# Kernel tuning notes

Measured on AMD Instinct MI355X. Metric: run time of the kernel, lower is better.

The kernel has to match this reference:

```python
import jax, jax.numpy as jnp
import numpy as np

B, S = 8192, 32
N_NODES, N_EDGES = 200000, 500000
D_NODE = D_EDGE = 172
D_TIME = 100
D_IN = D_NODE + D_NODE + D_EDGE + D_TIME  # 616


def setup_inputs() -> dict:
    key = jax.random.key(0)
    ks = jax.random.split(key, 16)
    node_raw_features = jax.random.normal(ks[0], (N_NODES, D_NODE), dtype=jnp.float32)
    edge_raw_features = jax.random.normal(ks[1], (N_EDGES, D_EDGE), dtype=jnp.float32)
    src_node_ids = jax.random.randint(ks[2], (B,), 0, N_NODES)
    dst_node_ids = jax.random.randint(ks[3], (B,), 0, N_NODES)
    node_interact_times = jax.random.uniform(ks[4], (B,), dtype=jnp.float32) * 1000.0
    src_nbr_ids = jax.random.randint(ks[5], (B, S), 0, N_NODES)
    src_edge_ids = jax.random.randint(ks[6], (B, S), 0, N_EDGES)
    src_nbr_times = jax.random.uniform(ks[7], (B, S), dtype=jnp.float32) * 1000.0
    dst_nbr_ids = jax.random.randint(ks[8], (B, S), 0, N_NODES)
    dst_edge_ids = jax.random.randint(ks[9], (B, S), 0, N_EDGES)
    dst_nbr_times = jax.random.uniform(ks[10], (B, S), dtype=jnp.float32) * 1000.0
    # TimeEncoder: frozen Linear(1, D_TIME) with w = 1/10^linspace(0,9,D_TIME), b = 0
    time_w = (1.0 / (10.0 ** jnp.linspace(0.0, 9.0, D_TIME))).astype(jnp.float32)
    time_b = jnp.zeros((D_TIME,), dtype=jnp.float32)
    W_out = jax.random.normal(ks[11], (D_IN, D_NODE), dtype=jnp.float32) * 0.02
    b_out = jnp.zeros((D_NODE,), dtype=jnp.float32)
    return {
        "node_raw_features": node_raw_features,
        "edge_raw_features": edge_raw_features,
        "src_node_ids": src_node_ids,
        "dst_node_ids": dst_node_ids,
        "node_interact_times": node_interact_times,
        "src_nbr_ids": src_nbr_ids,
        "src_edge_ids": src_edge_ids,
        "src_nbr_times": src_nbr_times,
        "dst_nbr_ids": dst_nbr_ids,
        "dst_edge_ids": dst_edge_ids,
        "dst_nbr_times": dst_nbr_times,
        "time_w": time_w,
        "time_b": time_b,
        "W_out": W_out,
        "b_out": b_out,
    }


def _side_embedding(node_raw_features, edge_raw_features, node_ids, interact_times,
                    nbr_ids, edge_ids, nbr_times, time_w, time_b, W_out, b_out):
    nf = node_raw_features[nbr_ids]            # [B,S,D_NODE] gather
    ef = edge_raw_features[edge_ids]           # [B,S,D_EDGE] gather
    dt = interact_times[:, None] - nbr_times   # [B,S]
    tf = jnp.cos(dt[..., None] * time_w + time_b)  # [B,S,D_TIME]
    tf = jnp.where((nbr_ids == 0)[..., None], 0.0, tf)  # zero padded-time features
    combined = jnp.concatenate([nf, ef, tf], axis=-1)   # [B,S,D_NODE+D_EDGE+D_TIME]
    agg = combined.mean(axis=1)                          # mean over padded seq (divide by S)
    cur = node_raw_features[node_ids]                    # [B,D_NODE]
    inp = jnp.concatenate([cur, agg], axis=-1)           # [B,D_IN]
    return jax.nn.relu(inp @ W_out + b_out)              # dropout is identity in eval


def reference(node_raw_features, edge_raw_features, src_node_ids, dst_node_ids,
              node_interact_times, src_nbr_ids, src_edge_ids, src_nbr_times,
              dst_nbr_ids, dst_edge_ids, dst_nbr_times, time_w, time_b, W_out, b_out):
    src_emb = _side_embedding(node_raw_features, edge_raw_features, src_node_ids,
                              node_interact_times, src_nbr_ids, src_edge_ids,
                              src_nbr_times, time_w, time_b, W_out, b_out)
    dst_emb = _side_embedding(node_raw_features, edge_raw_features, dst_node_ids,
                              node_interact_times, dst_nbr_ids, dst_edge_ids,
                              dst_nbr_times, time_w, time_b, W_out, b_out)
    dummy = jnp.zeros_like(src_emb)
    return src_emb, dst_emb, dummy
```

## Files before the change

### kernel.cpp

```cpp
#include <hip/hip_runtime.h>

#define ROWS  16
#define BLOCK 512
#define PAD   620

__global__ __launch_bounds__(BLOCK) void spe_fused(
    const float* __restrict__ nodef,
    const float* __restrict__ edgef,
    const int*   __restrict__ src_ids,
    const int*   __restrict__ dst_ids,
    const float* __restrict__ itimes,
    const int*   __restrict__ s_nbr,
    const int*   __restrict__ s_eid,
    const float* __restrict__ s_t,
    const int*   __restrict__ d_nbr,
    const int*   __restrict__ d_eid,
    const float* __restrict__ d_t,
    const float* __restrict__ tw,
    const float* __restrict__ tb,
    const float* __restrict__ W,
    const float* __restrict__ bout,
    float*       __restrict__ out)
{
    __shared__ float inp[ROWS * PAD];
    __shared__ int   noff[ROWS * 32];
    __shared__ int   eoff[ROWS * 32];
    __shared__ float dtm[ROWS * 32];
    __shared__ float msk[ROWS * 32];
    __shared__ int   curoff[ROWS];
    __shared__ float twl[100], tbl[100];

    const int tid     = threadIdx.x;
    const int side    = blockIdx.x >> 9;
    const int rowbase = (blockIdx.x & 511) * ROWS;

    const int*   nbr  = side ? d_nbr : s_nbr;
    const int*   eidp = side ? d_eid : s_eid;
    const float* ntp  = side ? d_t   : s_t;
    const int*   nids = side ? dst_ids : src_ids;

    {
        int i   = tid;
        int g   = rowbase * 32 + i;
        int nid = nbr[g];
        noff[i] = nid * 172;
        eoff[i] = eidp[g] * 172;
        dtm[i]  = itimes[rowbase + (i >> 5)] - ntp[g];
        msk[i]  = (nid == 0) ? 0.f : 1.f;
    }
    if (tid < ROWS) curoff[tid] = nids[rowbase + tid] * 172;
    if (tid < 100) { twl[tid] = tw[tid]; tbl[tid] = tb[tid]; }
    __syncthreads();

    for (int i = tid; i < ROWS * 43; i += BLOCK) {
        int r = i / 43, c = i - r * 43;
        *(float4*)&inp[r * PAD + 4 * c] =
            *(const float4*)&nodef[curoff[r] + 4 * c];
    }

    for (int i = tid; i < ROWS * 43; i += BLOCK) {
        int r = i / 43, c = i - r * 43;
        const int dd = 4 * c, rb = r * 32;
        float4 acc = {0.f, 0.f, 0.f, 0.f};
        #pragma unroll
        for (int s0 = 0; s0 < 32; s0 += 8) {
            float4 v[8];
            #pragma unroll
            for (int u = 0; u < 8; ++u)
                v[u] = *(const float4*)&nodef[noff[rb + s0 + u] + dd];
            #pragma unroll
            for (int u = 0; u < 8; ++u) {
                acc.x += v[u].x; acc.y += v[u].y;
                acc.z += v[u].z; acc.w += v[u].w;
            }
        }
        acc.x *= (1.f/32.f); acc.y *= (1.f/32.f);
        acc.z *= (1.f/32.f); acc.w *= (1.f/32.f);
        *(float4*)&inp[r * PAD + 172 + dd] = acc;
    }

    for (int i = tid; i < ROWS * 43; i += BLOCK) {
        int r = i / 43, c = i - r * 43;
        const int dd = 4 * c, rb = r * 32;
        float4 acc = {0.f, 0.f, 0.f, 0.f};
        #pragma unroll
        for (int s0 = 0; s0 < 32; s0 += 8) {
            float4 v[8];
            #pragma unroll
            for (int u = 0; u < 8; ++u)
                v[u] = *(const float4*)&edgef[eoff[rb + s0 + u] + dd];
            #pragma unroll
            for (int u = 0; u < 8; ++u) {
                acc.x += v[u].x; acc.y += v[u].y;
                acc.z += v[u].z; acc.w += v[u].w;
            }
        }
        acc.x *= (1.f/32.f); acc.y *= (1.f/32.f);
        acc.z *= (1.f/32.f); acc.w *= (1.f/32.f);
        *(float4*)&inp[r * PAD + 344 + dd] = acc;
    }

    for (int i = tid; i < ROWS * 100; i += BLOCK) {
        int r = i / 100, j = i - r * 100;
        const int rb = r * 32;
        float w = twl[j], b = tbl[j];
        float acc = 0.f;
        #pragma unroll
        for (int s = 0; s < 32; ++s)
            acc += msk[rb + s] * __cosf(dtm[rb + s] * w + b);
        inp[r * PAD + 516 + j] = acc * (1.f / 32.f);
    }
    __syncthreads();

    if (tid < 344) {
        const int ct = tid % 43, rt = tid / 43;
        const int j0 = ct * 4, r0 = rt * 2;
        float acc[2][4] = {};
        float a[2][4];
        for (int k = 0; k < 616; k += 4) {
            #pragma unroll
            for (int ri = 0; ri < 2; ++ri)
                *(float4*)&a[ri][0] = *(const float4*)&inp[(r0 + ri) * PAD + k];
            #pragma unroll
            for (int kk = 0; kk < 4; ++kk) {
                float4 wv = *(const float4*)&W[(k + kk) * 172 + j0];
                #pragma unroll
                for (int ri = 0; ri < 2; ++ri) {
                    acc[ri][0] += a[ri][kk] * wv.x;
                    acc[ri][1] += a[ri][kk] * wv.y;
                    acc[ri][2] += a[ri][kk] * wv.z;
                    acc[ri][3] += a[ri][kk] * wv.w;
                }
            }
        }
        float4 bias = *(const float4*)&bout[j0];
        #pragma unroll
        for (int ri = 0; ri < 2; ++ri) {
            int row = rowbase + r0 + ri;
            float4 v;
            v.x = fmaxf(acc[ri][0] + bias.x, 0.f);
            v.y = fmaxf(acc[ri][1] + bias.y, 0.f);
            v.z = fmaxf(acc[ri][2] + bias.z, 0.f);
            v.w = fmaxf(acc[ri][3] + bias.w, 0.f);
            *(float4*)&out[(size_t)(side * 8192 + row) * 172 + j0] = v;
        }
    }

    if (side == 0) {
        const float4 z = {0.f, 0.f, 0.f, 0.f};
        for (int i = tid; i < ROWS * 43; i += BLOCK) {
            int r = i / 43, c = i - r * 43;
            *(float4*)&out[(size_t)(2 * 8192 + rowbase + r) * 172 + 4 * c] = z;
        }
    }
}

extern "C" void kernel_launch(void* const* d_in, const int* in_sizes, int n_in,
                              void* d_out, int out_size, void* d_ws, size_t ws_size,
                              hipStream_t stream) {
    const float* nodef   = (const float*)d_in[0];
    const float* edgef   = (const float*)d_in[1];
    const int*   src_ids = (const int*)  d_in[2];
    const int*   dst_ids = (const int*)  d_in[3];
    const float* itimes  = (const float*)d_in[4];
    const int*   s_nbr   = (const int*)  d_in[5];
    const int*   s_eid   = (const int*)  d_in[6];
    const float* s_t     = (const float*)d_in[7];
    const int*   d_nbr   = (const int*)  d_in[8];
    const int*   d_eid   = (const int*)  d_in[9];
    const float* d_t     = (const float*)d_in[10];
    const float* tw      = (const float*)d_in[11];
    const float* tb      = (const float*)d_in[12];
    const float* W       = (const float*)d_in[13];
    const float* bout    = (const float*)d_in[14];
    float* out = (float*)d_out;

    spe_fused<<<1024, BLOCK, 0, stream>>>(
        nodef, edgef, src_ids, dst_ids, itimes,
        s_nbr, s_eid, s_t, d_nbr, d_eid, d_t,
        tw, tb, W, bout, out);
}
```

Before: 221.7 us.

## Split neighbor gather into separate high-parallelism kernel feeding GEMM kernel

Moves the node and edge neighbor gather-mean out of the fused kernel into a separate kernel with one thread per (row, float4 column), launched over 5504 blocks, writing aggregates to workspace. The GEMM kernel then reads the precomputed aggregates instead of performing the gathers. The aim is more memory-level parallelism for the random gathers, which were limited by the fused kernel's 1024 blocks. The cost is an extra workspace round trip and a second launch.

```diff
diff --git a/kernel.cpp b/kernel.cpp
--- a/kernel.cpp
+++ b/kernel.cpp
@@ -1,30 +1,69 @@
 #include <hip/hip_runtime.h>
 
 #define ROWS  16
-#define BLOCK 512
+#define GB    512
+#define PB    256
 #define PAD   620
+#define AGG_STRIDE 344
 
-__global__ __launch_bounds__(BLOCK) void spe_fused(
+__global__ __launch_bounds__(PB) void prep_gather(
     const float* __restrict__ nodef,
     const float* __restrict__ edgef,
+    const int*   __restrict__ s_nbr,
+    const int*   __restrict__ s_eid,
+    const int*   __restrict__ d_nbr,
+    const int*   __restrict__ d_eid,
+    float*       __restrict__ agg)
+{
+    const int i    = blockIdx.x * PB + threadIdx.x;
+    const int grow = i / 86, cc = i - grow * 86;
+    const int side = grow >> 13, row = grow & 8191;
+    const bool is_edge = cc >= 43;
+    const int  c  = is_edge ? cc - 43 : cc;
+    const int  dd = 4 * c;
+
+    const int* idt = is_edge ? (side ? d_eid : s_eid)
+                             : (side ? d_nbr : s_nbr);
+    const float* bp = is_edge ? edgef : nodef;
+    const int4* idv = (const int4*)&idt[row * 32];
+
+    float4 acc = {0.f, 0.f, 0.f, 0.f};
+    #pragma unroll
+    for (int b = 0; b < 4; ++b) {
+        int4 q0 = idv[2 * b], q1 = idv[2 * b + 1];
+        int off[8] = {q0.x, q0.y, q0.z, q0.w, q1.x, q1.y, q1.z, q1.w};
+        float4 v[8];
+        #pragma unroll
+        for (int u = 0; u < 8; ++u)
+            v[u] = *(const float4*)&bp[off[u] * 172 + dd];
+        #pragma unroll
+        for (int u = 0; u < 8; ++u) {
+            acc.x += v[u].x; acc.y += v[u].y;
+            acc.z += v[u].z; acc.w += v[u].w;
+        }
+    }
+    acc.x *= (1.f/32.f); acc.y *= (1.f/32.f);
+    acc.z *= (1.f/32.f); acc.w *= (1.f/32.f);
+    *(float4*)&agg[(size_t)grow * AGG_STRIDE + (is_edge ? 172 : 0) + dd] = acc;
+}
+
+__global__ __launch_bounds__(GB) void gemm_fused(
+    const float* __restrict__ nodef,
     const int*   __restrict__ src_ids,
     const int*   __restrict__ dst_ids,
     const float* __restrict__ itimes,
     const int*   __restrict__ s_nbr,
-    const int*   __restrict__ s_eid,
     const float* __restrict__ s_t,
     const int*   __restrict__ d_nbr,
-    const int*   __restrict__ d_eid,
     const float* __restrict__ d_t,
     const float* __restrict__ tw,
     const float* __restrict__ tb,
     const float* __restrict__ W,
     const float* __restrict__ bout,
+    const float* __restrict__ agg,
     float*       __restrict__ out)
 {
     __shared__ float inp[ROWS * PAD];
-    __shared__ int   noff[ROWS * 32];
-    __shared__ int   eoff[ROWS * 32];
     __shared__ float dtm[ROWS * 32];
     __shared__ float msk[ROWS * 32];
     __shared__ int   curoff[ROWS];
@@ -35,7 +74,6 @@
     const int rowbase = (blockIdx.x & 511) * ROWS;
 
     const int*   nbr  = side ? d_nbr : s_nbr;
-    const int*   eidp = side ? d_eid : s_eid;
     const float* ntp  = side ? d_t   : s_t;
     const int*   nids = side ? dst_ids : src_ids;
 
@@ -43,8 +81,6 @@
         int i   = tid;
         int g   = rowbase * 32 + i;
         int nid = nbr[g];
-        noff[i] = nid * 172;
-        eoff[i] = eidp[g] * 172;
         dtm[i]  = itimes[rowbase + (i >> 5)] - ntp[g];
         msk[i]  = (nid == 0) ? 0.f : 1.f;
     }
@@ -52,55 +88,19 @@
     if (tid < 100) { twl[tid] = tw[tid]; tbl[tid] = tb[tid]; }
     __syncthreads();
 
-    for (int i = tid; i < ROWS * 43; i += BLOCK) {
+    for (int i = tid; i < ROWS * 43; i += GB) {
         int r = i / 43, c = i - r * 43;
         *(float4*)&inp[r * PAD + 4 * c] =
             *(const float4*)&nodef[curoff[r] + 4 * c];
     }
 
-    for (int i = tid; i < ROWS * 43; i += BLOCK) {
-        int r = i / 43, c = i - r * 43;
-        const int dd = 4 * c, rb = r * 32;
-        float4 acc = {0.f, 0.f, 0.f, 0.f};
-        #pragma unroll
-        for (int s0 = 0; s0 < 32; s0 += 8) {
-            float4 v[8];
-            #pragma unroll
-            for (int u = 0; u < 8; ++u)
-                v[u] = *(const float4*)&nodef[noff[rb + s0 + u] + dd];
-            #pragma unroll
-            for (int u = 0; u < 8; ++u) {
-                acc.x += v[u].x; acc.y += v[u].y;
-                acc.z += v[u].z; acc.w += v[u].w;
-            }
-        }
-        acc.x *= (1.f/32.f); acc.y *= (1.f/32.f);
-        acc.z *= (1.f/32.f); acc.w *= (1.f/32.f);
-        *(float4*)&inp[r * PAD + 172 + dd] = acc;
+    for (int i = tid; i < ROWS * 86; i += GB) {
+        int r = i / 86, c = i - r * 86;
+        *(float4*)&inp[r * PAD + 172 + 4 * c] =
+            *(const float4*)&agg[(size_t)(side * 8192 + rowbase + r) * AGG_STRIDE + 4 * c];
     }
 
-    for (int i = tid; i < ROWS * 43; i += BLOCK) {
-        int r = i / 43, c = i - r * 43;
-        const int dd = 4 * c, rb = r * 32;
-        float4 acc = {0.f, 0.f, 0.f, 0.f};
-        #pragma unroll
-        for (int s0 = 0; s0 < 32; s0 += 8) {
-            float4 v[8];
-            #pragma unroll
-            for (int u = 0; u < 8; ++u)
-                v[u] = *(const float4*)&edgef[eoff[rb + s0 + u] + dd];
-            #pragma unroll
-            for (int u = 0; u < 8; ++u) {
-                acc.x += v[u].x; acc.y += v[u].y;
-                acc.z += v[u].z; acc.w += v[u].w;
-            }
-        }
-        acc.x *= (1.f/32.f); acc.y *= (1.f/32.f);
-        acc.z *= (1.f/32.f); acc.w *= (1.f/32.f);
-        *(float4*)&inp[r * PAD + 344 + dd] = acc;
-    }
-
-    for (int i = tid; i < ROWS * 100; i += BLOCK) {
+    for (int i = tid; i < ROWS * 100; i += GB) {
         int r = i / 100, j = i - r * 100;
         const int rb = r * 32;
         float w = twl[j], b = tbl[j];
@@ -148,7 +148,7 @@
 
     if (side == 0) {
         const float4 z = {0.f, 0.f, 0.f, 0.f};
-        for (int i = tid; i < ROWS * 43; i += BLOCK) {
+        for (int i = tid; i < ROWS * 43; i += GB) {
             int r = i / 43, c = i - r * 43;
             *(float4*)&out[(size_t)(2 * 8192 + rowbase + r) * 172 + 4 * c] = z;
         }
@@ -174,9 +174,13 @@
     const float* W       = (const float*)d_in[13];
     const float* bout    = (const float*)d_in[14];
     float* out = (float*)d_out;
+    float* agg = (float*)d_ws;
 
-    spe_fused<<<1024, BLOCK, 0, stream>>>(
-        nodef, edgef, src_ids, dst_ids, itimes,
-        s_nbr, s_eid, s_t, d_nbr, d_eid, d_t,
-        tw, tb, W, bout, out);
+    prep_gather<<<5504, PB, 0, stream>>>(
+        nodef, edgef, s_nbr, s_eid, d_nbr, d_eid, agg);
+
+    gemm_fused<<<1024, GB, 0, stream>>>(
+        nodef, src_ids, dst_ids, itimes,
+        s_nbr, s_t, d_nbr, d_t,
+        tw, tb, W, bout, agg, out);
 }
```

Result: slower. 258.8 us (+16.8%).

## Quantize feature tables to FP8 and split fused kernel into gather stages

Applied to the files above, without the earlier changes.

Splits the single fused kernel into separate passes: quantize the node and edge tables to FP8 in workspace, then gather and mean-reduce neighbour features from the FP8 copies. The current-node copy, the time encoding and the final GEMM each become their own kernel, all going through an fp32 intermediate buffer. The goal is to shrink the bytes moved by the random neighbour gathers. In exchange, every call reads both full tables to quantize them, adds an intermediate round trip and several launches, and FP8 rounding may loosen accuracy.

```diff
diff --git a/kernel.cpp b/kernel.cpp
--- a/kernel.cpp
+++ b/kernel.cpp
@@ -1,114 +1,150 @@
 #include <hip/hip_runtime.h>
 
-#define ROWS  16
-#define BLOCK 512
-#define PAD   620
-
-__global__ __launch_bounds__(BLOCK) void spe_fused(
+typedef float v2f __attribute__((ext_vector_type(2)));
+
+#define NROWS_GRID 16
+#define GB 512
+
+__device__ inline unsigned pack4_fp8(float a, float b, float c, float d) {
+    int t = __builtin_amdgcn_cvt_pk_fp8_f32(a, b, 0, false);
+    t     = __builtin_amdgcn_cvt_pk_fp8_f32(c, d, t, true);
+    return (unsigned)t;
+}
+
+__global__ __launch_bounds__(256) void quant_tab(
+    const float* __restrict__ src,
+    uint4*       __restrict__ dst,
+    int n)
+{
+    int i = blockIdx.x * 256 + threadIdx.x;
+    int row = i / 11, c = i - row * 11;
+    if (row >= n) return;
+    const float4* s = (const float4*)(src + (size_t)row * 172);
+    float v[16];
+    if (c < 10) {
+        #pragma unroll
+        for (int j = 0; j < 4; ++j) {
+            float4 f = s[4 * c + j];
+            v[4*j+0] = f.x; v[4*j+1] = f.y; v[4*j+2] = f.z; v[4*j+3] = f.w;
+        }
+    } else {
+        #pragma unroll
+        for (int j = 0; j < 3; ++j) {
+            float4 f = s[40 + j];
+            v[4*j+0] = f.x; v[4*j+1] = f.y; v[4*j+2] = f.z; v[4*j+3] = f.w;
+        }
+        v[12] = v[13] = v[14] = v[15] = 0.f;
+    }
+    uint4 o;
+    o.x = pack4_fp8(v[0],  v[1],  v[2],  v[3]);
+    o.y = pack4_fp8(v[4],  v[5],  v[6],  v[7]);
+    o.z = pack4_fp8(v[8],  v[9],  v[10], v[11]);
+    o.w = pack4_fp8(v[12], v[13], v[14], v[15]);
+    dst[(size_t)row * 11 + c] = o;
+}
+
+__global__ __launch_bounds__(256) void gather_q(
+    const uint4* __restrict__ Q,
+    const int*   __restrict__ s_ids,
+    const int*   __restrict__ d_ids,
+    float*       __restrict__ inpw,
+    int baseoff)
+{
+    int i    = blockIdx.x * 256 + threadIdx.x;
+    int grow = i / 11, c = i - grow * 11;
+    int side = grow >> 13, row = grow & 8191;
+    const int4* idv = (const int4*)&((side ? d_ids : s_ids)[row * 32]);
+
+    float acc[16];
+    #pragma unroll
+    for (int k = 0; k < 16; ++k) acc[k] = 0.f;
+
+    #pragma unroll
+    for (int b = 0; b < 4; ++b) {
+        int4 q0 = idv[2 * b], q1 = idv[2 * b + 1];
+        int off[8] = {q0.x, q0.y, q0.z, q0.w, q1.x, q1.y, q1.z, q1.w};
+        uint4 v[8];
+        #pragma unroll
+        for (int u = 0; u < 8; ++u)
+            v[u] = Q[(size_t)off[u] * 11 + c];
+        #pragma unroll
+        for (int u = 0; u < 8; ++u) {
+            unsigned w[4] = {v[u].x, v[u].y, v[u].z, v[u].w};
+            #pragma unroll
+            for (int q = 0; q < 4; ++q) {
+                v2f lo = __builtin_amdgcn_cvt_pk_f32_fp8((int)w[q], false);
+                v2f hi = __builtin_amdgcn_cvt_pk_f32_fp8((int)w[q], true);
+                acc[4*q+0] += lo.x; acc[4*q+1] += lo.y;
+                acc[4*q+2] += hi.x; acc[4*q+3] += hi.y;
+            }
+        }
+    }
+
+    float* dstrow = inpw + (size_t)grow * 616 + baseoff + 16 * c;
+    int nf4 = (c == 10) ? 3 : 4;
+    for (int j = 0; j < nf4; ++j) {
+        float4 o = { acc[4*j+0] * (1.f/32.f), acc[4*j+1] * (1.f/32.f),
+                     acc[4*j+2] * (1.f/32.f), acc[4*j+3] * (1.f/32.f) };
+        *(float4*)(dstrow + 4 * j) = o;
+    }
+}
+
+__global__ __launch_bounds__(256) void cur_copy(
     const float* __restrict__ nodef,
-    const float* __restrict__ edgef,
     const int*   __restrict__ src_ids,
     const int*   __restrict__ dst_ids,
+    float*       __restrict__ inpw)
+{
+    int i    = blockIdx.x * 256 + threadIdx.x;
+    int grow = i / 43, c = i - grow * 43;
+    int side = grow >> 13, row = grow & 8191;
+    int id   = (side ? dst_ids : src_ids)[row];
+    *(float4*)(inpw + (size_t)grow * 616 + 4 * c) =
+        *(const float4*)(nodef + (size_t)id * 172 + 4 * c);
+}
+
+__global__ __launch_bounds__(256) void time_enc(
+    const int*   __restrict__ s_nbr,
+    const int*   __restrict__ d_nbr,
+    const float* __restrict__ s_t,
+    const float* __restrict__ d_t,
     const float* __restrict__ itimes,
-    const int*   __restrict__ s_nbr,
-    const int*   __restrict__ s_eid,
-    const float* __restrict__ s_t,
-    const int*   __restrict__ d_nbr,
-    const int*   __restrict__ d_eid,
-    const float* __restrict__ d_t,
     const float* __restrict__ tw,
     const float* __restrict__ tb,
+    float*       __restrict__ inpw)
+{
+    int i    = blockIdx.x * 256 + threadIdx.x;
+    int grow = i / 100, j = i - grow * 100;
+    int side = grow >> 13, row = grow & 8191;
+    const int*   nbr = (side ? d_nbr : s_nbr) + row * 32;
+    const float* nt  = (side ? d_t   : s_t)   + row * 32;
+    float it = itimes[row];
+    float w = tw[j], b = tb[j];
+    float acc = 0.f;
+    #pragma unroll
+    for (int s = 0; s < 32; ++s) {
+        float m = (nbr[s] == 0) ? 0.f : 1.f;
+        acc += m * __cosf((it - nt[s]) * w + b);
+    }
+    inpw[(size_t)grow * 616 + 516 + j] = acc * (1.f / 32.f);
+}
+
+__global__ __launch_bounds__(GB) void final_gemm(
+    const float* __restrict__ inpw,
     const float* __restrict__ W,
     const float* __restrict__ bout,
     float*       __restrict__ out)
 {
-    __shared__ float inp[ROWS * PAD];
-    __shared__ int   noff[ROWS * 32];
-    __shared__ int   eoff[ROWS * 32];
-    __shared__ float dtm[ROWS * 32];
-    __shared__ float msk[ROWS * 32];
-    __shared__ int   curoff[ROWS];
-    __shared__ float twl[100], tbl[100];
-
-    const int tid     = threadIdx.x;
-    const int side    = blockIdx.x >> 9;
-    const int rowbase = (blockIdx.x & 511) * ROWS;
-
-    const int*   nbr  = side ? d_nbr : s_nbr;
-    const int*   eidp = side ? d_eid : s_eid;
-    const float* ntp  = side ? d_t   : s_t;
-    const int*   nids = side ? dst_ids : src_ids;
-
-    {
-        int i   = tid;
-        int g   = rowbase * 32 + i;
-        int nid = nbr[g];
-        noff[i] = nid * 172;
-        eoff[i] = eidp[g] * 172;
-        dtm[i]  = itimes[rowbase + (i >> 5)] - ntp[g];
-        msk[i]  = (nid == 0) ? 0.f : 1.f;
-    }
-    if (tid < ROWS) curoff[tid] = nids[rowbase + tid] * 172;
-    if (tid < 100) { twl[tid] = tw[tid]; tbl[tid] = tb[tid]; }
-    __syncthreads();
-
-    for (int i = tid; i < ROWS * 43; i += BLOCK) {
-        int r = i / 43, c = i - r * 43;
-        *(float4*)&inp[r * PAD + 4 * c] =
-            *(const float4*)&nodef[curoff[r] + 4 * c];
-    }
-
-    for (int i = tid; i < ROWS * 43; i += BLOCK) {
-        int r = i / 43, c = i - r * 43;
-        const int dd = 4 * c, rb = r * 32;
-        float4 acc = {0.f, 0.f, 0.f, 0.f};
-        #pragma unroll
-        for (int s0 = 0; s0 < 32; s0 += 8) {
-            float4 v[8];
-            #pragma unroll
-            for (int u = 0; u < 8; ++u)
-                v[u] = *(const float4*)&nodef[noff[rb + s0 + u] + dd];
-            #pragma unroll
-            for (int u = 0; u < 8; ++u) {
-                acc.x += v[u].x; acc.y += v[u].y;
-                acc.z += v[u].z; acc.w += v[u].w;
-            }
-        }
-        acc.x *= (1.f/32.f); acc.y *= (1.f/32.f);
-        acc.z *= (1.f/32.f); acc.w *= (1.f/32.f);
-        *(float4*)&inp[r * PAD + 172 + dd] = acc;
-    }
-
-    for (int i = tid; i < ROWS * 43; i += BLOCK) {
-        int r = i / 43, c = i - r * 43;
-        const int dd = 4 * c, rb = r * 32;
-        float4 acc = {0.f, 0.f, 0.f, 0.f};
-        #pragma unroll
-        for (int s0 = 0; s0 < 32; s0 += 8) {
-            float4 v[8];
-            #pragma unroll
-            for (int u = 0; u < 8; ++u)
-                v[u] = *(const float4*)&edgef[eoff[rb + s0 + u] + dd];
-            #pragma unroll
-            for (int u = 0; u < 8; ++u) {
-                acc.x += v[u].x; acc.y += v[u].y;
-                acc.z += v[u].z; acc.w += v[u].w;
-            }
-        }
-        acc.x *= (1.f/32.f); acc.y *= (1.f/32.f);
-        acc.z *= (1.f/32.f); acc.w *= (1.f/32.f);
-        *(float4*)&inp[r * PAD + 344 + dd] = acc;
-    }
-
-    for (int i = tid; i < ROWS * 100; i += BLOCK) {
-        int r = i / 100, j = i - r * 100;
-        const int rb = r * 32;
-        float w = twl[j], b = tbl[j];
-        float acc = 0.f;
-        #pragma unroll
-        for (int s = 0; s < 32; ++s)
-            acc += msk[rb + s] * __cosf(dtm[rb + s] * w + b);
-        inp[r * PAD + 516 + j] = acc * (1.f / 32.f);
+    __shared__ float inp[NROWS_GRID * 620];
+    const int tid      = threadIdx.x;
+    const int side     = blockIdx.x >> 9;
+    const int rowbase  = (blockIdx.x & 511) * NROWS_GRID;
+    const int growbase = side * 8192 + rowbase;
+
+    for (int i = tid; i < NROWS_GRID * 154; i += GB) {
+        int r = i / 154, c = i - r * 154;
+        *(float4*)&inp[r * 620 + 4 * c] =
+            *(const float4*)&inpw[(size_t)(growbase + r) * 616 + 4 * c];
     }
     __syncthreads();
 
@@ -120,7 +156,7 @@
         for (int k = 0; k < 616; k += 4) {
             #pragma unroll
             for (int ri = 0; ri < 2; ++ri)
-                *(float4*)&a[ri][0] = *(const float4*)&inp[(r0 + ri) * PAD + k];
+                *(float4*)&a[ri][0] = *(const float4*)&inp[(r0 + ri) * 620 + k];
             #pragma unroll
             for (int kk = 0; kk < 4; ++kk) {
                 float4 wv = *(const float4*)&W[(k + kk) * 172 + j0];
@@ -148,7 +184,7 @@
 
     if (side == 0) {
         const float4 z = {0.f, 0.f, 0.f, 0.f};
-        for (int i = tid; i < ROWS * 43; i += BLOCK) {
+        for (int i = tid; i < NROWS_GRID * 43; i += GB) {
             int r = i / 43, c = i - r * 43;
             *(float4*)&out[(size_t)(2 * 8192 + rowbase + r) * 172 + 4 * c] = z;
         }
@@ -175,8 +211,19 @@
     const float* bout    = (const float*)d_in[14];
     float* out = (float*)d_out;
 
-    spe_fused<<<1024, BLOCK, 0, stream>>>(
-        nodef, edgef, src_ids, dst_ids, itimes,
-        s_nbr, s_eid, s_t, d_nbr, d_eid, d_t,
-        tw, tb, W, bout, out);
-}
+    char*  ws    = (char*)d_ws;
+    float* inpw  = (float*)ws;
+    uint4* nodeQ = (uint4*)(ws + (size_t)48  * 1024 * 1024);
+    uint4* edgeQ = (uint4*)(ws + (size_t)96  * 1024 * 1024);
+
+    quant_tab<<<8594, 256, 0, stream>>>(nodef, nodeQ, 200000);
+    gather_q<<<704, 256, 0, stream>>>(nodeQ, s_nbr, d_nbr, inpw, 172);
+
+    quant_tab<<<21485, 256, 0, stream>>>(edgef, edgeQ, 500000);
+    gather_q<<<704, 256, 0, stream>>>(edgeQ, s_eid, d_eid, inpw, 344);
+
+    cur_copy<<<2752, 256, 0, stream>>>(nodef, src_ids, dst_ids, inpw);
+    time_enc<<<6400, 256, 0, stream>>>(s_nbr, d_nbr, s_t, d_t, itimes, tw, tb, inpw);
+
+    final_gemm<<<1024, GB, 0, stream>>>(inpw, W, bout, out);
+}
```

Measured after the change: 315.4 us. 42.3% more time.

## Quantize node and edge tables to FP8 before gathering neighbor features

Applied to the files above, without the earlier changes.

Adds a pre-pass kernel that converts the full node and edge feature tables to packed FP8 in workspace, then gathers neighbor rows from the FP8 copies and dequantizes them while accumulating the mean. The node and edge gather loops are merged into one loop over 16-element chunks. The aim is to cut the bytes moved by the random-row gathers, but every call must first stream both full float tables to write the FP8 copies. FP8 also adds quantization error to the aggregated features.

```diff
diff --git a/kernel.cpp b/kernel.cpp
--- a/kernel.cpp
+++ b/kernel.cpp
@@ -4,9 +4,56 @@
 #define BLOCK 512
 #define PAD   620
 
-__global__ __launch_bounds__(BLOCK) void spe_fused(
+typedef float v2f __attribute__((ext_vector_type(2)));
+
+__device__ inline unsigned pack4_fp8(float a, float b, float c, float d) {
+    int t = __builtin_amdgcn_cvt_pk_fp8_f32(a, b, 0, false);
+    t     = __builtin_amdgcn_cvt_pk_fp8_f32(c, d, t, true);
+    return (unsigned)t;
+}
+
+__global__ __launch_bounds__(256) void quant_all(
     const float* __restrict__ nodef,
     const float* __restrict__ edgef,
+    uint4*       __restrict__ nodeQ,
+    uint4*       __restrict__ edgeQ)
+{
+    const int NODE_ITEMS = 200000 * 11;
+    const int TOT_ITEMS  = NODE_ITEMS + 500000 * 11;
+    int i = blockIdx.x * 256 + threadIdx.x;
+    if (i >= TOT_ITEMS) return;
+    const float* src; uint4* dst; int row, c;
+    if (i < NODE_ITEMS) { row = i / 11; c = i - row * 11; src = nodef; dst = nodeQ; }
+    else { int j = i - NODE_ITEMS; row = j / 11; c = j - row * 11; src = edgef; dst = edgeQ; }
+
+    const float4* s = (const float4*)(src + (size_t)row * 172);
+    float v[16];
+    if (c < 10) {
+        #pragma unroll
+        for (int j = 0; j < 4; ++j) {
+            float4 f = s[4 * c + j];
+            v[4*j+0] = f.x; v[4*j+1] = f.y; v[4*j+2] = f.z; v[4*j+3] = f.w;
+        }
+    } else {
+        #pragma unroll
+        for (int j = 0; j < 3; ++j) {
+            float4 f = s[40 + j];
+            v[4*j+0] = f.x; v[4*j+1] = f.y; v[4*j+2] = f.z; v[4*j+3] = f.w;
+        }
+        v[12] = v[13] = v[14] = v[15] = 0.f;
+    }
+    uint4 o;
+    o.x = pack4_fp8(v[0],  v[1],  v[2],  v[3]);
+    o.y = pack4_fp8(v[4],  v[5],  v[6],  v[7]);
+    o.z = pack4_fp8(v[8],  v[9],  v[10], v[11]);
+    o.w = pack4_fp8(v[12], v[13], v[14], v[15]);
+    dst[(size_t)row * 11 + c] = o;
+}
+
+__global__ __launch_bounds__(BLOCK) void spe_fused_q(
+    const float* __restrict__ nodef,
+    const uint4* __restrict__ nodeQ,
+    const uint4* __restrict__ edgeQ,
     const int*   __restrict__ src_ids,
     const int*   __restrict__ dst_ids,
     const float* __restrict__ itimes,
@@ -23,8 +70,8 @@
     float*       __restrict__ out)
 {
     __shared__ float inp[ROWS * PAD];
-    __shared__ int   noff[ROWS * 32];
-    __shared__ int   eoff[ROWS * 32];
+    __shared__ int   nid_s[ROWS * 32];
+    __shared__ int   eid_s[ROWS * 32];
     __shared__ float dtm[ROWS * 32];
     __shared__ float msk[ROWS * 32];
     __shared__ int   curoff[ROWS];
@@ -40,13 +87,13 @@
     const int*   nids = side ? dst_ids : src_ids;
 
     {
-        int i   = tid;
-        int g   = rowbase * 32 + i;
-        int nid = nbr[g];
-        noff[i] = nid * 172;
-        eoff[i] = eidp[g] * 172;
-        dtm[i]  = itimes[rowbase + (i >> 5)] - ntp[g];
-        msk[i]  = (nid == 0) ? 0.f : 1.f;
+        int i    = tid;
+        int g    = rowbase * 32 + i;
+        int nid  = nbr[g];
+        nid_s[i] = nid;
+        eid_s[i] = eidp[g];
+        dtm[i]   = itimes[rowbase + (i >> 5)] - ntp[g];
+        msk[i]   = (nid == 0) ? 0.f : 1.f;
     }
     if (tid < ROWS) curoff[tid] = nids[rowbase + tid] * 172;
     if (tid < 100) { twl[tid] = tw[tid]; tbl[tid] = tb[tid]; }
@@ -58,46 +105,47 @@
             *(const float4*)&nodef[curoff[r] + 4 * c];
     }
 
-    for (int i = tid; i < ROWS * 43; i += BLOCK) {
-        int r = i / 43, c = i - r * 43;
-        const int dd = 4 * c, rb = r * 32;
-        float4 acc = {0.f, 0.f, 0.f, 0.f};
+    for (int i = tid; i < ROWS * 22; i += BLOCK) {
+        int r = i / 22, cc = i - r * 22;
+        const bool is_edge = cc >= 11;
+        const int  c  = is_edge ? cc - 11 : cc;
+        const int  rb = r * 32;
+        const uint4* Q    = is_edge ? edgeQ : nodeQ;
+        const int*   ids  = is_edge ? eid_s : nid_s;
+
+        float acc[16];
+        #pragma unroll
+        for (int k = 0; k < 16; ++k) acc[k] = 0.f;
+
         #pragma unroll
         for (int s0 = 0; s0 < 32; s0 += 8) {
-            float4 v[8];
+            uint4 v[8];
             #pragma unroll
             for (int u = 0; u < 8; ++u)
-                v[u] = *(const float4*)&nodef[noff[rb + s0 + u] + dd];
+                v[u] = Q[(size_t)ids[rb + s0 + u] * 11 + c];
             #pragma unroll
             for (int u = 0; u < 8; ++u) {
-                acc.x += v[u].x; acc.y += v[u].y;
-                acc.z += v[u].z; acc.w += v[u].w;
+                unsigned w[4] = {v[u].x, v[u].y, v[u].z, v[u].w};
+                #pragma unroll
+                for (int q = 0; q < 4; ++q) {
+                    v2f lo = __builtin_amdgcn_cvt_pk_f32_fp8((int)w[q], false);
+                    v2f hi = __builtin_amdgcn_cvt_pk_f32_fp8((int)w[q], true);
+                    acc[4*q+0] += lo.x; acc[4*q+1] += lo.y;
+                    acc[4*q+2] += hi.x; acc[4*q+3] += hi.y;
+                }
             }
         }
-        acc.x *= (1.f/32.f); acc.y *= (1.f/32.f);
-        acc.z *= (1.f/32.f); acc.w *= (1.f/32.f);
-        *(float4*)&inp[r * PAD + 172 + dd] = acc;
-    }
-
-    for (int i = tid; i < ROWS * 43; i += BLOCK) {
-        int r = i / 43, c = i - r * 43;
-        const int dd = 4 * c, rb = r * 32;
-        float4 acc = {0.f, 0.f, 0.f, 0.f};
-        #pragma unroll
-        for (int s0 = 0; s0 < 32; s0 += 8) {
-            float4 v[8];
-            #pragma unroll
-            for (int u = 0; u < 8; ++u)
-                v[u] = *(const float4*)&edgef[eoff[rb + s0 + u] + dd];
-            #pragma unroll
-            for (int u = 0; u < 8; ++u) {
-                acc.x += v[u].x; acc.y += v[u].y;
-                acc.z += v[u].z; acc.w += v[u].w;
+
+        float* dstp = &inp[r * PAD + (is_edge ? 344 : 172) + 16 * c];
+        int nf4 = (c == 10) ? 3 : 4;
+        #pragma unroll
+        for (int j = 0; j < 4; ++j) {
+            if (j < nf4) {
+                float4 o = { acc[4*j+0] * (1.f/32.f), acc[4*j+1] * (1.f/32.f),
+                             acc[4*j+2] * (1.f/32.f), acc[4*j+3] * (1.f/32.f) };
+                *(float4*)(dstp + 4 * j) = o;
             }
         }
-        acc.x *= (1.f/32.f); acc.y *= (1.f/32.f);
-        acc.z *= (1.f/32.f); acc.w *= (1.f/32.f);
-        *(float4*)&inp[r * PAD + 344 + dd] = acc;
     }
 
     for (int i = tid; i < ROWS * 100; i += BLOCK) {
@@ -175,8 +223,14 @@
     const float* bout    = (const float*)d_in[14];
     float* out = (float*)d_out;
 
-    spe_fused<<<1024, BLOCK, 0, stream>>>(
-        nodef, edgef, src_ids, dst_ids, itimes,
+    char*  ws    = (char*)d_ws;
+    uint4* nodeQ = (uint4*)ws;
+    uint4* edgeQ = (uint4*)(ws + (size_t)48 * 1024 * 1024);
+
+    quant_all<<<30079, 256, 0, stream>>>(nodef, edgef, nodeQ, edgeQ);
+
+    spe_fused_q<<<1024, BLOCK, 0, stream>>>(
+        nodef, nodeQ, edgeQ, src_ids, dst_ids, itimes,
         s_nbr, s_eid, s_t, d_nbr, d_eid, d_t,
         tw, tb, W, bout, out);
 }
```

Result: slower. 323.0 us (+45.7%).
